# Performance work log

Hardware: AMD Instinct MI355X
Metric: run time of the kernel (lower is better)

The kernel has to match this reference:

```python
import jax, jax.numpy as jnp
import numpy as np


def setup_inputs() -> dict:
    key = jax.random.key(0)
    ks = jax.random.split(key, 11)
    B, n, d_x, d = 8, 2048, 128, 512
    H, hd = 8, 64  # num_heads, head_size = d_v // num_heads
    std_key = d ** -0.5      # d_k ** -0.5 (d_k = 512 after mlp rep)
    std_val = d ** -0.5      # d_v ** -0.5
    return {
        "x1": jax.random.normal(ks[0], (B, n, d_x), jnp.float32),
        "x2": jax.random.normal(ks[1], (B, n, d_x), jnp.float32),
        "r": jax.random.normal(ks[2], (B, n, d), jnp.float32),
        # BatchLinear (shared mlp rep): d_x -> 512 -> 512
        "W1": jax.random.normal(ks[3], (d_x, d), jnp.float32) * (d_x ** -0.5),
        "b1": jnp.zeros((d,), jnp.float32),
        "W2": jax.random.normal(ks[4], (d, d), jnp.float32) * (d ** -0.5),
        "b2": jnp.zeros((d,), jnp.float32),
        # per-head 1x1-conv projections, stacked over heads: [H, out, in]
        "Wq": jax.random.normal(ks[5], (H, hd, d), jnp.float32) * std_key,
        "Wk": jax.random.normal(ks[6], (H, hd, d), jnp.float32) * std_key,
        "Wv": jax.random.normal(ks[7], (H, hd, d), jnp.float32) * std_key,
        "Wo": jax.random.normal(ks[8], (H, d, hd), jnp.float32) * std_val,
    }


def reference(x1, x2, r, W1, b1, W2, b2, Wq, Wk, Wv, Wo):
    # rep == 'mlp': shared BatchLinear applied to x1 (keys) and x2 (queries)
    def mlp(x):  # [B,n,d_x] -> [B,n,512]; relu on all but last layer
        h = jax.nn.relu(jnp.einsum("bnd,de->bne", x, W1) + b1)
        return jnp.einsum("bnd,de->bne", h, W2) + b2

    k = mlp(x1)  # [B,n1,d_k]
    q = mlp(x2)  # [B,n2,d_k]

    # multihead: per-head 1x1 convs == linear projections; batched over heads
    qh = jnp.einsum("bmd,hed->bhme", q, Wq)  # [B,H,m,hd]
    kh = jnp.einsum("bnd,hed->bhne", k, Wk)  # [B,H,n,hd]
    vh = jnp.einsum("bnd,hed->bhne", r, Wv)  # [B,H,n,hd]

    scale = jnp.sqrt(jnp.asarray(qh.shape[-1], qh.dtype))
    scores = jnp.einsum("bhme,bhne->bhmn", qh, kh) / scale
    w = jax.nn.softmax(scores, axis=-1)      # normalise=True
    o = jnp.einsum("bhmn,bhne->bhme", w, vh)  # [B,H,m,hd]

    # per-head output conv (hd -> d_v), summed over heads
    rep = jnp.einsum("bhme,hde->bmd", o, Wo)  # [B,m,d_v]
    return rep
```

## Files before the change

### kernel.cpp

```cpp
#include <hip/hip_runtime.h>
#include <stdint.h>

typedef __attribute__((ext_vector_type(8))) short short8;
typedef __attribute__((ext_vector_type(4))) float f32x4;
typedef __attribute__((ext_vector_type(16))) float f32x16;
typedef __attribute__((ext_vector_type(4))) unsigned u32x4;

#define DEVINL __device__ __forceinline__

DEVINL unsigned short f2bf(float f) {
  unsigned u = __float_as_uint(f);
  u = (u + 0x7FFFu + ((u >> 16) & 1u)) >> 16;
  return (unsigned short)u;
}

DEVINL void gload_lds16(const void* g, void* lds) {
  __builtin_amdgcn_global_load_lds(
      (const __attribute__((address_space(1))) unsigned int*)g,
      (__attribute__((address_space(3))) unsigned int*)lds, 16, 0, 0);
}

DEVINL float fexp2(float x) {
  float r;
  asm("v_exp_f32 %0, %1" : "=v"(r) : "v"(x));
  return r;
}

DEVINL unsigned cvtpk(float lo, float hi) {
  unsigned r;
  asm("v_cvt_pk_bf16_f32 %0, %1, %2" : "=v"(r) : "v"(lo), "v"(hi));
  return r;
}

DEVINL void pl32swap(unsigned& a, unsigned& b) {
  asm("v_permlane32_swap_b32 %0, %1" : "+v"(a), "+v"(b));
}


__global__ void cvt_wquad(const float* __restrict__ W2, const float* __restrict__ Wq,
                          const float* __restrict__ Wk, const float* __restrict__ Wv,
                          unsigned short* __restrict__ W2B, unsigned short* __restrict__ WqB,
                          unsigned short* __restrict__ WkB, unsigned short* __restrict__ WvB) {
  const int a = blockIdx.x >> 8;
  const int i = (blockIdx.x & 255) * 256 + threadIdx.x;
  const float* src = (a == 0) ? W2 : (a == 1) ? Wq : (a == 2) ? Wk : Wv;
  unsigned short* dst = (a == 0) ? W2B : (a == 1) ? WqB : (a == 2) ? WkB : WvB;
  const float scale = (a == 1) ? 0.18033688f : 1.0f;
  float4 v = ((const float4*)src)[i];
  ushort4 o;
  o.x = f2bf(v.x * scale); o.y = f2bf(v.y * scale);
  o.z = f2bf(v.z * scale); o.w = f2bf(v.w * scale);
  ((ushort4*)dst)[i] = o;
}

__global__ void prep_misc(const float* __restrict__ W1, const float* __restrict__ Wo,
                          const float* __restrict__ b2, const float* __restrict__ Wq,
                          const float* __restrict__ Wk,
                          unsigned short* __restrict__ W1T, unsigned short* __restrict__ WoT,
                          float* __restrict__ bqf, float* __restrict__ bkf) {
  const int bid = blockIdx.x, tid = threadIdx.x;
  if (bid < 256) {
    int idx = bid * 256 + tid;
    int n = idx >> 7, k = idx & 127;
    W1T[idx] = f2bf(W1[(size_t)k * 512 + n]);
  } else if (bid < 1280) {
    int idx = (bid - 256) * 256 + tid;
    int d = idx >> 9, j = idx & 511, h = j >> 6, e = j & 63;
    WoT[idx] = f2bf(Wo[(size_t)h * 32768 + (size_t)d * 64 + e]);
  } else {
    int rid = (bid - 1280) * 4 + (tid >> 6);
    int l = tid & 63;
    int e = rid & 511, which = rid >> 9;
    const float* W = which ? Wk : Wq;
    float scale = which ? 1.0f : 0.18033688f;
    float acc = 0.f;
#pragma unroll
    for (int j = 0; j < 8; ++j)
      acc += b2[l * 8 + j] * W[(size_t)e * 512 + l * 8 + j];
    acc *= scale;
#pragma unroll
    for (int off = 1; off < 64; off <<= 1) acc += __shfl_xor(acc, off, 64);
    if (l == 0) (which ? bkf : bqf)[e] = acc;
  }
}

__global__ void cvt_all(const float* __restrict__ x1, const float* __restrict__ x2,
                        const float* __restrict__ r,
                        unsigned short* __restrict__ Xb, unsigned short* __restrict__ Rb) {
  const int bid = blockIdx.x, tid = threadIdx.x;
  const float* src;
  unsigned short* dst;
  int i;
  if (bid < 2048)      { src = x1; dst = Xb;           i = bid * 256 + tid; }
  else if (bid < 4096) { src = x2; dst = Xb + 2097152; i = (bid - 2048) * 256 + tid; }
  else                 { src = r;  dst = Rb;           i = (bid - 4096) * 256 + tid; }
  float4 v = ((const float4*)src)[i];
  ushort4 o;
  o.x = f2bf(v.x); o.y = f2bf(v.y); o.z = f2bf(v.z); o.w = f2bf(v.w);
  ((ushort4*)dst)[i] = o;
}

__global__ __launch_bounds__(256) void v_transpose(const unsigned short* __restrict__ VH,
                                                   unsigned short* __restrict__ VT) {
  const int bh = blockIdx.x, t = blockIdx.y;
  const int b = bh >> 3, h = bh & 7;
  __shared__ __align__(16) unsigned short L[128 * 72];
  const int tid = threadIdx.x;
#pragma unroll
  for (int i = 0; i < 4; ++i) {
    int c = i * 256 + tid, kk = c >> 3, cr = c & 7;
    *(short8*)&L[kk * 72 + cr * 8] =
        *(const short8*)&VH[(size_t)(b * 2048 + t * 128 + kk) * 512 + h * 64 + cr * 8];
  }
  __syncthreads();
#pragma unroll
  for (int i = 0; i < 4; ++i) {
    int c = i * 256 + tid, e = c >> 4, ckn = c & 15;
    short8 v;
#pragma unroll
    for (int j = 0; j < 8; ++j) v[j] = L[(ckn * 8 + j) * 72 + e];
    *(short8*)&VT[((size_t)bh * 64 + e) * 2048 + t * 128 + ckn * 8] = v;
  }
}

template <bool RELU, typename TOut>
__global__ __launch_bounds__(256) void gemm64(
    const unsigned short* A0, const unsigned short* B0, const float* bias0, TOut* C0,
    const unsigned short* A1, const unsigned short* B1, const float* bias1, TOut* C1,
    const unsigned short* A2, const unsigned short* B2, const float* bias2, TOut* C2,
    int M, int N, int K) {
  __shared__ __align__(16) char smem[32768];
  unsigned short* As = (unsigned short*)smem;
  unsigned short* Bs = (unsigned short*)(smem + 16384);

  const int z = blockIdx.z;
  const unsigned short* A = (z == 0) ? A0 : (z == 1) ? A1 : A2;
  const unsigned short* Bt = (z == 0) ? B0 : (z == 1) ? B1 : B2;
  const float* bias = (z == 0) ? bias0 : (z == 1) ? bias1 : bias2;
  TOut* C = (z == 0) ? C0 : (z == 1) ? C1 : C2;

  const int nx = gridDim.x;
  int id = blockIdx.y * nx + blockIdx.x;
  const int nwg = nx * gridDim.y;
  if ((nwg & 7) == 0) id = (id & 7) * (nwg >> 3) + (id >> 3);
  const int n0 = (id % nx) * 128, m0 = (id / nx) * 128;

  const int tid = threadIdx.x, w = tid >> 6, l = tid & 63;
  const int wm = w >> 1, wn = w & 1;
  const int lr = l & 15, lg = l >> 4;

  f32x4 zero4 = {0.f, 0.f, 0.f, 0.f};
  f32x4 acc[4][4];
#pragma unroll
  for (int i = 0; i < 4; ++i)
#pragma unroll
    for (int j = 0; j < 4; ++j) acc[i][j] = zero4;

  for (int k0 = 0; k0 < K; k0 += 64) {
#pragma unroll
    for (int i = 0; i < 4; ++i) {
      const int c = i * 256 + tid;
      const int row = c >> 3, ch = c & 7;
      const int sl = (ch ^ (row & 7)) * 8;
      gload_lds16(A + (size_t)(m0 + row) * K + k0 + sl, (char*)As + c * 16);
      gload_lds16(Bt + (size_t)(n0 + row) * K + k0 + sl, (char*)Bs + c * 16);
    }
    asm volatile("s_waitcnt vmcnt(0)" ::: "memory");
    __syncthreads();

#pragma unroll
    for (int kk = 0; kk < 2; ++kk) {
      short8 af[4], bfr[4];
#pragma unroll
      for (int mi = 0; mi < 4; ++mi) {
        const int row = wm * 64 + mi * 16 + lr;
        af[mi] = *(const short8*)((const char*)As + row * 128 + (((kk * 4 + lg) ^ (row & 7)) * 16));
      }
#pragma unroll
      for (int ni = 0; ni < 4; ++ni) {
        const int row = wn * 64 + ni * 16 + lr;
        bfr[ni] = *(const short8*)((const char*)Bs + row * 128 + (((kk * 4 + lg) ^ (row & 7)) * 16));
      }
#pragma unroll
      for (int mi = 0; mi < 4; ++mi)
#pragma unroll
        for (int ni = 0; ni < 4; ++ni)
          acc[mi][ni] = __builtin_amdgcn_mfma_f32_16x16x32_bf16(af[mi], bfr[ni], acc[mi][ni], 0, 0, 0);
    }
    __syncthreads();
  }

#pragma unroll
  for (int ni = 0; ni < 4; ++ni) {
    const int col = n0 + wn * 64 + ni * 16 + lr;
    const float bv = bias ? bias[col] : 0.f;
#pragma unroll
    for (int mi = 0; mi < 4; ++mi) {
      const int row = m0 + wm * 64 + mi * 16 + lg * 4;
#pragma unroll
      for (int r = 0; r < 4; ++r) {
        float v = acc[mi][ni][r] + bv;
        if (RELU) v = fmaxf(v, 0.f);
        if constexpr (sizeof(TOut) == 2)
          C[(size_t)(row + r) * N + col] = (TOut)f2bf(v);
        else
          C[(size_t)(row + r) * N + col] = v;
      }
    }
  }
}

DEVINL void stage_kv(const unsigned short* Kp, const unsigned short* Vp,
                     char* kb, char* vb, int tid, int k0) {
  const int row = tid >> 3, cs = tid & 7;
  const int sl = (cs ^ (row & 7)) * 8;
  gload_lds16(Kp + (size_t)(k0 + row) * 512 + sl, kb + tid * 16);
  gload_lds16(Vp + (size_t)row * 2048 + k0 + sl, vb + tid * 16);
}

__global__ __launch_bounds__(512, 2) void attn_sw2(
    const unsigned short* __restrict__ Q, const unsigned short* __restrict__ Kh,
    const unsigned short* __restrict__ VT, unsigned short* __restrict__ O) {
  const int bh = blockIdx.x, b = bh >> 3, h = bh & 7;
  const int q0 = blockIdx.y * 512;
  const int tid = threadIdx.x, w = tid >> 6, l = tid & 63;
  const int lq = l & 31, hi = l >> 5;
  const size_t baseBH = (size_t)b * 2048 * 512 + (size_t)h * 64;

  __shared__ __align__(16) char smem[49152];

  const unsigned short* Kp = Kh + baseBH;
  const unsigned short* Vp = VT + (size_t)bh * 64 * 2048;

  short8 qf[2][4];
#pragma unroll
  for (int qb = 0; qb < 2; ++qb) {
    const unsigned short* qp =
        Q + baseBH + (size_t)(q0 + w * 64 + qb * 32 + lq) * 512 + hi * 8;
#pragma unroll
    for (int kc = 0; kc < 4; ++kc) qf[qb][kc] = *(const short8*)(qp + kc * 16);
  }

  f32x16 ot[2][2];
#pragma unroll
  for (int qb = 0; qb < 2; ++qb)
#pragma unroll
    for (int eh = 0; eh < 2; ++eh)
#pragma unroll
      for (int r = 0; r < 16; ++r) ot[qb][eh][r] = 0.f;
  float m_run[2] = {-1e30f, -1e30f}, l_run[2] = {0.f, 0.f};
  const int xs = (lq & 7);

  stage_kv(Kp, Vp, smem, smem + 24576, tid, 0);
  stage_kv(Kp, Vp, smem + 8192, smem + 24576 + 8192, tid, 64);

  for (int t = 0; t < 32; ++t) {
    if (t < 31) asm volatile("s_waitcnt vmcnt(2)" ::: "memory");
    else        asm volatile("s_waitcnt vmcnt(0)" ::: "memory");
    __builtin_amdgcn_s_barrier();
    if (t < 30) {
      const int tn = t + 2, rb = tn - (tn / 3) * 3;
      stage_kv(Kp, Vp, smem + rb * 8192, smem + 24576 + rb * 8192, tid, tn * 64);
    }
    const int cb = t - (t / 3) * 3;
    const char* klc = smem + cb * 8192;
    const char* vtc = smem + 24576 + cb * 8192;

    short8 kf[8];
#pragma unroll
    for (int kc = 0; kc < 4; ++kc)
#pragma unroll
      for (int kh = 0; kh < 2; ++kh)
        kf[kc * 2 + kh] =
            *(const short8*)(klc + (kh * 32 + lq) * 128 + (((kc * 2 + hi) ^ xs) * 16));

    short8 pfk[2][4];
#pragma unroll
    for (int qb = 0; qb < 2; ++qb) {
      f32x16 st0, st1;
#pragma unroll
      for (int r = 0; r < 16; ++r) { st0[r] = 0.f; st1[r] = 0.f; }
      __builtin_amdgcn_s_setprio(1);
#pragma unroll
      for (int kc = 0; kc < 4; ++kc) {
        st0 = __builtin_amdgcn_mfma_f32_32x32x16_bf16(kf[kc * 2 + 0], qf[qb][kc], st0, 0, 0, 0);
        st1 = __builtin_amdgcn_mfma_f32_32x32x16_bf16(kf[kc * 2 + 1], qf[qb][kc], st1, 0, 0, 0);
      }
      __builtin_amdgcn_s_setprio(0);

      float t8[8];
#pragma unroll
      for (int r = 0; r < 8; ++r)
        t8[r] = fmaxf(fmaxf(st0[r], st0[r + 8]), fmaxf(st1[r], st1[r + 8]));
      float mt = fmaxf(fmaxf(fmaxf(t8[0], t8[1]), fmaxf(t8[2], t8[3])),
                       fmaxf(fmaxf(t8[4], t8[5]), fmaxf(t8[6], t8[7])));
      mt = fmaxf(mt, __shfl_xor(mt, 32, 64));

      if (__any(mt > m_run[qb] + 8.0f)) {
        float mn = fmaxf(m_run[qb], mt);
        float al = fexp2(m_run[qb] - mn);
        m_run[qb] = mn;
        l_run[qb] *= al;
#pragma unroll
        for (int r = 0; r < 16; ++r) { ot[qb][0][r] *= al; ot[qb][1][r] *= al; }
      }
#pragma unroll
      for (int r = 0; r < 16; ++r) {
        st0[r] = fexp2(st0[r] - m_run[qb]);
        st1[r] = fexp2(st1[r] - m_run[qb]);
      }
      float s8[8];
#pragma unroll
      for (int r = 0; r < 8; ++r)
        s8[r] = (st0[r] + st0[r + 8]) + (st1[r] + st1[r + 8]);
      float rs = ((s8[0] + s8[1]) + (s8[2] + s8[3])) + ((s8[4] + s8[5]) + (s8[6] + s8[7]));
      rs += __shfl_xor(rs, 32, 64);
      l_run[qb] += rs;

#pragma unroll
      for (int kc = 0; kc < 4; ++kc) {
        const int c = kc & 1;
        float p0, p1, p2, p3, p4, p5, p6, p7;
        if (kc < 2) {
          p0 = st0[8*c+0]; p1 = st0[8*c+1]; p2 = st0[8*c+2]; p3 = st0[8*c+3];
          p4 = st0[8*c+4]; p5 = st0[8*c+5]; p6 = st0[8*c+6]; p7 = st0[8*c+7];
        } else {
          p0 = st1[8*c+0]; p1 = st1[8*c+1]; p2 = st1[8*c+2]; p3 = st1[8*c+3];
          p4 = st1[8*c+4]; p5 = st1[8*c+5]; p6 = st1[8*c+6]; p7 = st1[8*c+7];
        }
        unsigned X0 = cvtpk(p0, p1), X1 = cvtpk(p2, p3);
        unsigned Y0 = cvtpk(p4, p5), Y1 = cvtpk(p6, p7);
        pl32swap(X0, Y0);
        pl32swap(X1, Y1);
        u32x4 u = {X0, X1, Y0, Y1};
        pfk[qb][kc] = __builtin_bit_cast(short8, u);
      }
    }

    short8 vf[8];
#pragma unroll
    for (int kc = 0; kc < 4; ++kc)
#pragma unroll
      for (int vh = 0; vh < 2; ++vh)
        vf[kc * 2 + vh] =
            *(const short8*)(vtc + (vh * 32 + lq) * 128 + (((kc * 2 + hi) ^ xs) * 16));

    __builtin_amdgcn_s_setprio(1);
#pragma unroll
    for (int qb = 0; qb < 2; ++qb)
#pragma unroll
      for (int kc = 0; kc < 4; ++kc) {
        ot[qb][0] = __builtin_amdgcn_mfma_f32_32x32x16_bf16(vf[kc * 2 + 0], pfk[qb][kc], ot[qb][0], 0, 0, 0);
        ot[qb][1] = __builtin_amdgcn_mfma_f32_32x32x16_bf16(vf[kc * 2 + 1], pfk[qb][kc], ot[qb][1], 0, 0, 0);
      }
    __builtin_amdgcn_s_setprio(0);
  }

  __syncthreads();

  unsigned short (*eps)[32][68] = (unsigned short (*)[32][68])smem;
#pragma unroll
  for (int qb = 0; qb < 2; ++qb) {
    const float rinv = 1.0f / l_run[qb];
#pragma unroll
    for (int r = 0; r < 16; ++r) {
      const int e = (r & 3) + 8 * (r >> 2) + 4 * hi;
      eps[w][lq][e] = f2bf(ot[qb][0][r] * rinv);
      eps[w][lq][e + 32] = f2bf(ot[qb][1][r] * rinv);
    }
    asm volatile("s_waitcnt lgkmcnt(0)" ::: "memory");
    __builtin_amdgcn_sched_barrier(0);
#pragma unroll
    for (int i = 0; i < 4; ++i) {
      const int qq = i * 8 + (l >> 3), e0 = (l & 7) * 8;
      short8 v = *(const short8*)&eps[w][qq][e0];
      *(short8*)(O + baseBH + (size_t)(q0 + w * 64 + qb * 32 + qq) * 512 + e0) = v;
    }
    __builtin_amdgcn_sched_barrier(0);
  }
}


extern "C" void kernel_launch(void* const* d_in, const int* in_sizes, int n_in,
                              void* d_out, int out_size, void* d_ws, size_t ws_size,
                              hipStream_t stream) {
  const float* x1 = (const float*)d_in[0];
  const float* x2 = (const float*)d_in[1];
  const float* r  = (const float*)d_in[2];
  const float* W1 = (const float*)d_in[3];
  const float* b1 = (const float*)d_in[4];
  const float* W2 = (const float*)d_in[5];
  const float* b2 = (const float*)d_in[6];
  const float* Wq = (const float*)d_in[7];
  const float* Wk = (const float*)d_in[8];
  const float* Wv = (const float*)d_in[9];
  const float* Wo = (const float*)d_in[10];

  char* ws = (char*)d_ws;
  size_t off = 0;
  auto alloc = [&](size_t bytes) {
    char* p = ws + off;
    off = (off + bytes + 255) & ~(size_t)255;
    return p;
  };
  unsigned short* W1T = (unsigned short*)alloc(512 * 128 * 2);
  unsigned short* W2B = (unsigned short*)alloc(512 * 512 * 2);
  unsigned short* WqB = (unsigned short*)alloc(512 * 512 * 2);
  unsigned short* WkB = (unsigned short*)alloc(512 * 512 * 2);
  unsigned short* WvB = (unsigned short*)alloc(512 * 512 * 2);
  unsigned short* WoT = (unsigned short*)alloc(512 * 512 * 2);
  unsigned short* Fq  = (unsigned short*)alloc(512 * 512 * 2);
  unsigned short* Fk  = (unsigned short*)alloc(512 * 512 * 2);
  float* bqf = (float*)alloc(512 * 4);
  float* bkf = (float*)alloc(512 * 4);
  unsigned short* Xb  = (unsigned short*)alloc((size_t)32768 * 128 * 2);
  unsigned short* Hb  = (unsigned short*)alloc((size_t)32768 * 512 * 2);
  unsigned short* Rb  = (unsigned short*)alloc((size_t)16384 * 512 * 2);
  unsigned short* QHb = (unsigned short*)alloc((size_t)16384 * 512 * 2);
  unsigned short* KHb = (unsigned short*)alloc((size_t)16384 * 512 * 2);
  unsigned short* VHb = (unsigned short*)alloc((size_t)16384 * 512 * 2);
  unsigned short* VT  = Rb;
  unsigned short* Ob  = QHb;

  cvt_wquad<<<1024, 256, 0, stream>>>(W2, Wq, Wk, Wv, W2B, WqB, WkB, WvB);
  prep_misc<<<1536, 256, 0, stream>>>(W1, Wo, b2, Wq, Wk, W1T, WoT, bqf, bkf);
  gemm64<false, unsigned short><<<dim3(4, 4, 2), 256, 0, stream>>>(
      WqB, W2B, nullptr, Fq,  WkB, W2B, nullptr, Fk,  WkB, W2B, nullptr, Fk,
      512, 512, 512);
  cvt_all<<<12288, 256, 0, stream>>>(x1, x2, r, Xb, Rb);
  gemm64<true, unsigned short><<<dim3(4, 256, 1), 256, 0, stream>>>(
      Xb, W1T, b1, Hb,  Xb, W1T, b1, Hb,  Xb, W1T, b1, Hb,
      32768, 512, 128);
  gemm64<false, unsigned short><<<dim3(4, 128, 3), 256, 0, stream>>>(
      Hb, Fk, bkf, KHb,
      Hb + (size_t)16384 * 512, Fq, bqf, QHb,
      Rb, WvB, nullptr, VHb,
      16384, 512, 512);
  v_transpose<<<dim3(64, 16), 256, 0, stream>>>(VHb, VT);
  attn_sw2<<<dim3(64, 4), 512, 0, stream>>>(QHb, KHb, VT, Ob);
  gemm64<false, float><<<dim3(4, 128, 1), 256, 0, stream>>>(
      Ob, WoT, nullptr, (float*)d_out,  Ob, WoT, nullptr, (float*)d_out,
      Ob, WoT, nullptr, (float*)d_out,
      16384, 512, 512);
}
```

Before: 208.3 us.

## Shrink attention blocks to 256 threads and compute row sums with MFMA

The attention kernel now uses 256-thread blocks covering 256 queries each, so the grid doubles to 512 blocks. Each thread stages two K/V chunks per tile, and the vmcnt wait is raised to match. The softmax row-sum is no longer a VALU reduction plus cross-lane shuffle. It is accumulated by an MFMA against a ones vector, using the bf16-rounded probabilities. This moves work off the vector ALU and improves block count per CU. The cost is extra MFMA issue, an extra 16-register accumulator per query block, and twice as many K/V loads from global memory overall.

```diff
diff --git a/kernel.cpp b/kernel.cpp
--- a/kernel.cpp
+++ b/kernel.cpp
@@ -212,17 +212,21 @@
 
 DEVINL void stage_kv(const unsigned short* Kp, const unsigned short* Vp,
                      char* kb, char* vb, int tid, int k0) {
-  const int row = tid >> 3, cs = tid & 7;
-  const int sl = (cs ^ (row & 7)) * 8;
-  gload_lds16(Kp + (size_t)(k0 + row) * 512 + sl, kb + tid * 16);
-  gload_lds16(Vp + (size_t)row * 2048 + k0 + sl, vb + tid * 16);
-}
-
-__global__ __launch_bounds__(512, 2) void attn_sw2(
+#pragma unroll
+  for (int i = 0; i < 2; ++i) {
+    const int c = i * 256 + tid;
+    const int row = c >> 3, cs = c & 7;
+    const int sl = (cs ^ (row & 7)) * 8;
+    gload_lds16(Kp + (size_t)(k0 + row) * 512 + sl, kb + c * 16);
+    gload_lds16(Vp + (size_t)row * 2048 + k0 + sl, vb + c * 16);
+  }
+}
+
+__global__ __launch_bounds__(256, 2) void attn_sw3(
     const unsigned short* __restrict__ Q, const unsigned short* __restrict__ Kh,
     const unsigned short* __restrict__ VT, unsigned short* __restrict__ O) {
   const int bh = blockIdx.x, b = bh >> 3, h = bh & 7;
-  const int q0 = blockIdx.y * 512;
+  const int q0 = blockIdx.y * 256;
   const int tid = threadIdx.x, w = tid >> 6, l = tid & 63;
   const int lq = l & 31, hi = l >> 5;
   const size_t baseBH = (size_t)b * 2048 * 512 + (size_t)h * 64;
@@ -242,20 +246,21 @@
   }
 
   f32x16 ot[2][2];
-#pragma unroll
-  for (int qb = 0; qb < 2; ++qb)
-#pragma unroll
-    for (int eh = 0; eh < 2; ++eh)
-#pragma unroll
-      for (int r = 0; r < 16; ++r) ot[qb][eh][r] = 0.f;
-  float m_run[2] = {-1e30f, -1e30f}, l_run[2] = {0.f, 0.f};
+  f32x16 lt[2];
+#pragma unroll
+  for (int qb = 0; qb < 2; ++qb) {
+#pragma unroll
+    for (int r = 0; r < 16; ++r) { ot[qb][0][r] = 0.f; ot[qb][1][r] = 0.f; lt[qb][r] = 0.f; }
+  }
+  float m_run[2] = {-1e30f, -1e30f};
   const int xs = (lq & 7);
+  const short8 ones = {16256, 16256, 16256, 16256, 16256, 16256, 16256, 16256};
 
   stage_kv(Kp, Vp, smem, smem + 24576, tid, 0);
   stage_kv(Kp, Vp, smem + 8192, smem + 24576 + 8192, tid, 64);
 
   for (int t = 0; t < 32; ++t) {
-    if (t < 31) asm volatile("s_waitcnt vmcnt(2)" ::: "memory");
+    if (t < 31) asm volatile("s_waitcnt vmcnt(4)" ::: "memory");
     else        asm volatile("s_waitcnt vmcnt(0)" ::: "memory");
     __builtin_amdgcn_s_barrier();
     if (t < 30) {
@@ -300,7 +305,7 @@
         float mn = fmaxf(m_run[qb], mt);
         float al = fexp2(m_run[qb] - mn);
         m_run[qb] = mn;
-        l_run[qb] *= al;
+        lt[qb][0] *= al;
 #pragma unroll
         for (int r = 0; r < 16; ++r) { ot[qb][0][r] *= al; ot[qb][1][r] *= al; }
       }
@@ -309,13 +314,6 @@
         st0[r] = fexp2(st0[r] - m_run[qb]);
         st1[r] = fexp2(st1[r] - m_run[qb]);
       }
-      float s8[8];
-#pragma unroll
-      for (int r = 0; r < 8; ++r)
-        s8[r] = (st0[r] + st0[r + 8]) + (st1[r] + st1[r + 8]);
-      float rs = ((s8[0] + s8[1]) + (s8[2] + s8[3])) + ((s8[4] + s8[5]) + (s8[6] + s8[7]));
-      rs += __shfl_xor(rs, 32, 64);
-      l_run[qb] += rs;
 
 #pragma unroll
       for (int kc = 0; kc < 4; ++kc) {
@@ -334,6 +332,7 @@
         pl32swap(X1, Y1);
         u32x4 u = {X0, X1, Y0, Y1};
         pfk[qb][kc] = __builtin_bit_cast(short8, u);
+        lt[qb] = __builtin_amdgcn_mfma_f32_32x32x16_bf16(ones, pfk[qb][kc], lt[qb], 0, 0, 0);
       }
     }
 
@@ -361,7 +360,7 @@
   unsigned short (*eps)[32][68] = (unsigned short (*)[32][68])smem;
 #pragma unroll
   for (int qb = 0; qb < 2; ++qb) {
-    const float rinv = 1.0f / l_run[qb];
+    const float rinv = 1.0f / lt[qb][0];
 #pragma unroll
     for (int r = 0; r < 16; ++r) {
       const int e = (r & 3) + 8 * (r >> 2) + 4 * hi;
@@ -437,7 +436,7 @@
       Rb, WvB, nullptr, VHb,
       16384, 512, 512);
   v_transpose<<<dim3(64, 16), 256, 0, stream>>>(VHb, VT);
-  attn_sw2<<<dim3(64, 4), 512, 0, stream>>>(QHb, KHb, VT, Ob);
+  attn_sw3<<<dim3(64, 8), 256, 0, stream>>>(QHb, KHb, VT, Ob);
   gemm64<false, float><<<dim3(4, 128, 1), 256, 0, stream>>>(
       Ob, WoT, nullptr, (float*)d_out,  Ob, WoT, nullptr, (float*)d_out,
       Ob, WoT, nullptr, (float*)d_out,
```

After: 212.5 us. +2.0%, slower.
